# Optimization experiments

Hardware: AMD Instinct MI355X
Metric: run time of the kernel (lower is better)

Reference implementation:

```python
import jax, jax.numpy as jnp
import numpy as np

B, N_IMG, N_TXT = 8, 4096, 512
IMG_DIM, TEXT_DIM, H = 512, 768, 8
HD = IMG_DIM // H                      # 64, projection head dim
SCALE = (TEXT_DIM // H) ** -0.5        # module scales by text_head_dim^-0.5 (96)


def setup_inputs() -> dict:
    key = jax.random.key(0)
    ks = jax.random.split(key, 8)
    img_embeds = jax.random.normal(ks[0], (B, N_IMG, IMG_DIM), dtype=jnp.float32)
    text_embeds = jax.random.normal(ks[1], (B, N_TXT, TEXT_DIM), dtype=jnp.float32)
    text_attention_mask = jax.random.randint(ks[2], (B, N_TXT), 0, 2).astype(jnp.int32)
    s = 0.02
    Wq = jax.random.normal(ks[3], (IMG_DIM, IMG_DIM), dtype=jnp.float32) * s
    Wk = jax.random.normal(ks[4], (IMG_DIM, TEXT_DIM), dtype=jnp.float32) * s
    Wv = jax.random.normal(ks[5], (IMG_DIM, TEXT_DIM), dtype=jnp.float32) * s
    Wo = jax.random.normal(ks[6], (IMG_DIM, IMG_DIM), dtype=jnp.float32) * s
    bo = jnp.zeros((IMG_DIM,), dtype=jnp.float32)
    return {"img_embeds": img_embeds, "text_embeds": text_embeds,
            "text_attention_mask": text_attention_mask,
            "Wq": Wq, "Wk": Wk, "Wv": Wv, "Wo": Wo, "bo": bo}


def reference(img_embeds, text_embeds, text_attention_mask, Wq, Wk, Wv, Wo, bo):
    # projections (nn.Linear: x @ W.T), split into heads: (B, H, N, HD)
    q = (img_embeds @ Wq.T).reshape(B, N_IMG, H, HD).transpose(0, 2, 1, 3)
    k = (text_embeds @ Wk.T).reshape(B, N_TXT, H, HD).transpose(0, 2, 1, 3)
    v = (text_embeds @ Wv.T).reshape(B, N_TXT, H, HD).transpose(0, 2, 1, 3)
    # scores: (B, H, N_img, N_text)
    scores = jnp.einsum('bhid,bhjd->bhij', q, k) * SCALE
    mask = (text_attention_mask != 0)[:, None, None, :]  # (B,1,1,N_text)
    scores = jnp.where(mask, scores, -jnp.inf)
    probs = jax.nn.softmax(scores, axis=-1)
    attended = jnp.einsum('bhij,bhjd->bhid', probs, v)    # (B,H,N_img,HD)
    attended = attended.transpose(0, 2, 1, 3).reshape(B, N_IMG, IMG_DIM)
    return attended @ Wo.T + bo
```

## Files before the change

### kernel.cpp

```cpp
#include <hip/hip_runtime.h>
#include <hip/hip_bf16.h>
#include <cstdint>

#define NB   8
#define NIMG 4096
#define NTXT 512
#define DIMG 512
#define DTXT 768
#define NH   8
#define HD   64
#define SCALE 0.102062072615966f

typedef __attribute__((ext_vector_type(8))) short          s16x8;
typedef __attribute__((ext_vector_type(4))) unsigned short u16x4;
typedef __attribute__((ext_vector_type(4))) float          f32x4;
typedef unsigned short u16;
typedef unsigned int   u32;

union U8 { s16x8 v; u16 u[8]; };

__device__ __forceinline__ u16 f2bf(float f) {
  u32 u = __float_as_uint(f);
  u += 0x7fffu + ((u >> 16) & 1u);
  return (u16)(u >> 16);
}
__device__ __forceinline__ s16x8 cvt8(float4 a, float4 b) {
  U8 t;
  t.u[0]=f2bf(a.x); t.u[1]=f2bf(a.y); t.u[2]=f2bf(a.z); t.u[3]=f2bf(a.w);
  t.u[4]=f2bf(b.x); t.u[5]=f2bf(b.y); t.u[6]=f2bf(b.z); t.u[7]=f2bf(b.w);
  return t.v;
}

__global__ void convk(const float* __restrict__ in, u16* __restrict__ out, int n8) {
  int i = blockIdx.x * 256 + threadIdx.x;
  const int stride = gridDim.x * 256;
  for (; i < n8; i += stride) {
    float4 a = ((const float4*)in)[2 * i];
    float4 b = ((const float4*)in)[2 * i + 1];
    ((s16x8*)out)[i] = cvt8(a, b);
  }
}

__device__ __forceinline__ void gld16(const u16* g, u16* l) {
  __builtin_amdgcn_global_load_lds((const __attribute__((address_space(1))) u32*)g,
                                   (__attribute__((address_space(3))) u32*)l, 16, 0, 0);
}

template<int EPI, int NPER>
__global__ __launch_bounds__(256, 2)
void gemm_bf(const u16* __restrict__ A, const u16* __restrict__ W,
             const float* __restrict__ bias, void* __restrict__ Cp,
             const int N, const int K) {
  __shared__ u16 As[128 * 64];
  __shared__ u16 Bs[128 * 64];
  const int tid = threadIdx.x, lane = tid & 63, w = tid >> 6;
  const int l15 = lane & 15, l4 = lane >> 4;
  const int wm = (w >> 1) * 64, wn = (w & 1) * 64;
  const int m0 = blockIdx.y * 128, n0 = blockIdx.x * 128;
  const int srow = lane >> 3, schk = lane & 7;

  f32x4 acc[4][4] = {};

  for (int k0 = 0; k0 < K; k0 += 64) {
    __syncthreads();
#pragma unroll
    for (int i = 0; i < 4; ++i) {
      const int rg  = (w * 4 + i) * 8;
      const int row = rg + srow;
      const int sc  = schk ^ (row & 7);
      gld16(A + (size_t)(m0 + row) * K + k0 + sc * 8, &As[rg * 64]);
      gld16(W + (size_t)(n0 + row) * K + k0 + sc * 8, &Bs[rg * 64]);
    }
    __syncthreads();
#pragma unroll
    for (int ks = 0; ks < 2; ++ks) {
      s16x8 af[4], bw[4];
#pragma unroll
      for (int mf = 0; mf < 4; ++mf) {
        const int row = wm + mf * 16 + l15;
        af[mf] = *(const s16x8*)&As[row * 64 + (((ks * 4 + l4) ^ (row & 7)) << 3)];
      }
#pragma unroll
      for (int nf = 0; nf < 4; ++nf) {
        const int row = wn + nf * 16 + l15;
        bw[nf] = *(const s16x8*)&Bs[row * 64 + (((ks * 4 + l4) ^ (row & 7)) << 3)];
      }
#pragma unroll
      for (int mf = 0; mf < 4; ++mf)
#pragma unroll
        for (int nf = 0; nf < 4; ++nf)
          acc[mf][nf] = __builtin_amdgcn_mfma_f32_16x16x32_bf16(af[mf], bw[nf], acc[mf][nf], 0, 0, 0);
    }
  }

#pragma unroll
  for (int mf = 0; mf < 4; ++mf)
#pragma unroll
    for (int nf = 0; nf < 4; ++nf)
#pragma unroll
      for (int r = 0; r < 4; ++r) {
        const int grow = m0 + wm + mf * 16 + l4 * 4 + r;
        const int gcol = n0 + wn + nf * 16 + l15;
        const float v = acc[mf][nf][r];
        if constexpr (EPI == 2) {
          ((float*)Cp)[(size_t)grow * N + gcol] = v + bias[gcol];
        } else {
          const int bb = grow / NPER, nr = grow % NPER;
          const int hh = gcol >> 6, dd = gcol & 63;
          ((u16*)Cp)[((size_t)(bb * NH + hh) * NPER + nr) * HD + dd] = f2bf(v);
        }
      }
}

__global__ __launch_bounds__(256, 2)
void gemm_kv(const float* __restrict__ txt, const float* __restrict__ Wk,
             const float* __restrict__ Wv, u16* __restrict__ Kbf,
             u16* __restrict__ Vtw) {
  constexpr int K = DTXT;
  __shared__ u16 As[128 * 64];
  __shared__ u16 Bs[128 * 64];
  const int tid = threadIdx.x, lane = tid & 63, w = tid >> 6;
  const int l15 = lane & 15, l4 = lane >> 4;
  const int wm = (w >> 1) * 64, wn = (w & 1) * 64;
  const float* W = (blockIdx.x < 4) ? Wk : Wv;
  const int n0 = (blockIdx.x & 3) * 128;
  const int m0 = blockIdx.y * 128;

  f32x4 acc[4][4] = {};

  for (int k0 = 0; k0 < K; k0 += 64) {
    __syncthreads();
#pragma unroll
    for (int p = 0; p < 4; ++p) {
      const int q = tid + p * 256;
      const int row = q >> 3, c = q & 7;
      const int dst = row * 64 + ((c ^ (row & 7)) << 3);
      const float* sa = txt + (size_t)(m0 + row) * K + k0 + c * 8;
      *(s16x8*)&As[dst] = cvt8(*(const float4*)sa, *(const float4*)(sa + 4));
      const float* sw = W + (size_t)(n0 + row) * K + k0 + c * 8;
      *(s16x8*)&Bs[dst] = cvt8(*(const float4*)sw, *(const float4*)(sw + 4));
    }
    __syncthreads();
#pragma unroll
    for (int ks = 0; ks < 2; ++ks) {
      s16x8 af[4], bw[4];
#pragma unroll
      for (int mf = 0; mf < 4; ++mf) {
        const int row = wm + mf * 16 + l15;
        af[mf] = *(const s16x8*)&As[row * 64 + (((ks * 4 + l4) ^ (row & 7)) << 3)];
      }
#pragma unroll
      for (int nf = 0; nf < 4; ++nf) {
        const int row = wn + nf * 16 + l15;
        bw[nf] = *(const s16x8*)&Bs[row * 64 + (((ks * 4 + l4) ^ (row & 7)) << 3)];
      }
#pragma unroll
      for (int mf = 0; mf < 4; ++mf)
#pragma unroll
        for (int nf = 0; nf < 4; ++nf)
          acc[mf][nf] = __builtin_amdgcn_mfma_f32_16x16x32_bf16(af[mf], bw[nf], acc[mf][nf], 0, 0, 0);
    }
  }

#pragma unroll
  for (int mf = 0; mf < 4; ++mf)
#pragma unroll
    for (int nf = 0; nf < 4; ++nf)
#pragma unroll
      for (int r = 0; r < 4; ++r) {
        const int grow = m0 + wm + mf * 16 + l4 * 4 + r;
        const int gcol = n0 + wn + nf * 16 + l15;
        const int bb = grow >> 9, nr = grow & 511;
        const int hh = gcol >> 6, dd = gcol & 63;
        const u16 v = f2bf(acc[mf][nf][r]);
        if (blockIdx.x < 4)
          Kbf[((size_t)(bb * NH + hh) * NTXT + nr) * HD + dd] = v;
        else
          Vtw[((size_t)(bb * NH + hh) * HD + dd) * NTXT + nr] = v;
      }
}

__global__ __launch_bounds__(256, 2)
void attn_k(const u16* __restrict__ Qbf,
            const u16* __restrict__ Kbf,
            const u16* __restrict__ Vt,
            const int* __restrict__ msk,
            u16* __restrict__ Abf) {
  __shared__ u16 Plds[4][32 * 64];
  const int blk = blockIdx.x;
  const int qt = blk & 31, bh = blk >> 5;
  const int b = bh >> 3, h = bh & 7;
  const int tid = threadIdx.x, lane = tid & 63, w = tid >> 6;
  const int l15 = lane & 15, l4 = lane >> 4;
  const int sbase = lane & 48;

  const u16* Qb = Qbf + (size_t)bh * NIMG * HD;
  const u16* Kb = Kbf + (size_t)bh * NTXT * HD;
  const u16* Vb = Vt  + (size_t)bh * HD * NTXT;
  const int* mb = msk + b * NTXT;
  const int qrow0 = qt * 128 + w * 32;

  s16x8 aq[2][2];
#pragma unroll
  for (int nfq = 0; nfq < 2; ++nfq)
#pragma unroll
    for (int ks = 0; ks < 2; ++ks)
      aq[nfq][ks] = *(const s16x8*)(Qb + (size_t)(qrow0 + nfq * 16 + l15) * HD + ks * 32 + l4 * 8);

  f32x4 o[2][4] = {};
  float mst[2] = {-1e30f, -1e30f}, lst[2] = {0.f, 0.f};

  for (int t = 0; t < 8; ++t) {
    const int j0 = t * 64;
    s16x8 bk[4][2];
#pragma unroll
    for (int mfk = 0; mfk < 4; ++mfk)
#pragma unroll
      for (int ks = 0; ks < 2; ++ks)
        bk[mfk][ks] = *(const s16x8*)(Kb + (size_t)(j0 + mfk * 16 + l15) * HD + ks * 32 + l4 * 8);

    f32x4 st[4][2] = {};
#pragma unroll
    for (int ks = 0; ks < 2; ++ks)
#pragma unroll
      for (int mfk = 0; mfk < 4; ++mfk)
#pragma unroll
        for (int nfq = 0; nfq < 2; ++nfq)
          st[mfk][nfq] = __builtin_amdgcn_mfma_f32_16x16x32_bf16(bk[mfk][ks], aq[nfq][ks], st[mfk][nfq], 0, 0, 0);

    s16x8 bv[4][2];
#pragma unroll
    for (int hf = 0; hf < 4; ++hf)
#pragma unroll
      for (int ks = 0; ks < 2; ++ks)
        bv[hf][ks] = *(const s16x8*)(Vb + (size_t)(hf * 16 + l15) * NTXT + j0 + ks * 32 + l4 * 8);

    float madd[4][4];
#pragma unroll
    for (int mfk = 0; mfk < 4; ++mfk) {
      const int4 mm = *(const int4*)(mb + j0 + mfk * 16 + l4 * 4);
      madd[mfk][0] = mm.x ? 0.f : -1e30f;
      madd[mfk][1] = mm.y ? 0.f : -1e30f;
      madd[mfk][2] = mm.z ? 0.f : -1e30f;
      madd[mfk][3] = mm.w ? 0.f : -1e30f;
    }

#pragma unroll
    for (int nfq = 0; nfq < 2; ++nfq) {
      float nm = -1e30f;
#pragma unroll
      for (int mfk = 0; mfk < 4; ++mfk)
#pragma unroll
        for (int r = 0; r < 4; ++r) {
          const float sv = st[mfk][nfq][r] * SCALE + madd[mfk][r];
          st[mfk][nfq][r] = sv;
          nm = fmaxf(nm, sv);
        }
      nm = fmaxf(nm, __shfl_xor(nm, 16));
      nm = fmaxf(nm, __shfl_xor(nm, 32));
      const float mn = fmaxf(mst[nfq], nm);
      const float alpha = __expf(mst[nfq] - mn);
      mst[nfq] = mn;
      float ps = 0.f;
#pragma unroll
      for (int mfk = 0; mfk < 4; ++mfk)
#pragma unroll
        for (int r = 0; r < 4; ++r) {
          const float p = __expf(st[mfk][nfq][r] - mn);
          st[mfk][nfq][r] = p;
          ps += p;
        }
      ps += __shfl_xor(ps, 16);
      ps += __shfl_xor(ps, 32);
      lst[nfq] = lst[nfq] * alpha + ps;

      float ar[4];
#pragma unroll
      for (int r = 0; r < 4; ++r) ar[r] = __shfl(alpha, sbase + l4 * 4 + r);
#pragma unroll
      for (int hf = 0; hf < 4; ++hf)
#pragma unroll
        for (int r = 0; r < 4; ++r) o[nfq][hf][r] *= ar[r];

      const int q = nfq * 16 + l15;
      const int E = (q & 7) << 1;
#pragma unroll
      for (int mfk = 0; mfk < 4; ++mfk) {
        u16x4 pk;
        pk[0] = f2bf(st[mfk][nfq][0]); pk[1] = f2bf(st[mfk][nfq][1]);
        pk[2] = f2bf(st[mfk][nfq][2]); pk[3] = f2bf(st[mfk][nfq][3]);
        const int c8 = mfk * 4 + l4;
        *(u16x4*)((char*)&Plds[w][0] + q * 128 + (((c8) ^ E) << 3)) = pk;
      }
    }
    asm volatile("" ::: "memory");

#pragma unroll
    for (int mfq = 0; mfq < 2; ++mfq) {
      const int q = mfq * 16 + l15;
      const int E = (q & 7) << 1;
      s16x8 pa[2];
#pragma unroll
      for (int ks = 0; ks < 2; ++ks)
        pa[ks] = *(const s16x8*)((const char*)&Plds[w][0] + q * 128 + (((ks * 8 + l4 * 2) ^ E) << 3));
#pragma unroll
      for (int hf = 0; hf < 4; ++hf)
#pragma unroll
        for (int ks = 0; ks < 2; ++ks)
          o[mfq][hf] = __builtin_amdgcn_mfma_f32_16x16x32_bf16(pa[ks], bv[hf][ks], o[mfq][hf], 0, 0, 0);
    }
  }

#pragma unroll
  for (int nfq = 0; nfq < 2; ++nfq) {
    const float rl = 1.f / lst[nfq];
    float rr[4];
#pragma unroll
    for (int r = 0; r < 4; ++r) rr[r] = __shfl(rl, sbase + l4 * 4 + r);
#pragma unroll
    for (int hf = 0; hf < 4; ++hf)
#pragma unroll
      for (int r = 0; r < 4; ++r) {
        const int qrow = qrow0 + nfq * 16 + l4 * 4 + r;
        const int col = h * 64 + hf * 16 + l15;
        Abf[((size_t)b * NIMG + qrow) * DIMG + col] = f2bf(o[nfq][hf][r] * rr[r]);
      }
  }
}

extern "C" void kernel_launch(void* const* d_in, const int* in_sizes, int n_in,
                              void* d_out, int out_size, void* d_ws, size_t ws_size,
                              hipStream_t stream) {
  const float* img  = (const float*)d_in[0];
  const float* txt  = (const float*)d_in[1];
  const int*   mask = (const int*)d_in[2];
  const float* Wq   = (const float*)d_in[3];
  const float* Wk   = (const float*)d_in[4];
  const float* Wv   = (const float*)d_in[5];
  const float* Wo   = (const float*)d_in[6];
  const float* bo   = (const float*)d_in[7];
  float* out = (float*)d_out;

  char* ws = (char*)d_ws;
  u16* imgBf = (u16*)ws;
  u16* Qbf   = (u16*)(ws + 33554432);
  u16* Kbf   = (u16*)(ws + 67108864);
  u16* Vtw   = (u16*)(ws + 71303168);
  u16* WqBf  = (u16*)(ws + 75497472);
  u16* WoBf  = (u16*)(ws + 76021760);

  convk<<<2048, 256, 0, stream>>>(img, imgBf, NB * NIMG * DIMG / 8);
  convk<<<128,  256, 0, stream>>>(Wq, WqBf, DIMG * DIMG / 8);
  convk<<<128,  256, 0, stream>>>(Wo, WoBf, DIMG * DIMG / 8);

  gemm_bf<0, NIMG><<<dim3(4, 256), 256, 0, stream>>>(imgBf, WqBf, nullptr, Qbf, DIMG, DIMG);
  gemm_kv<<<dim3(8, 32), 256, 0, stream>>>(txt, Wk, Wv, Kbf, Vtw);
  attn_k<<<dim3(NB * NH * (NIMG / 128)), 256, 0, stream>>>(Qbf, Kbf, Vtw, mask, imgBf);
  gemm_bf<2, 1><<<dim3(4, 256), 256, 0, stream>>>(imgBf, WoBf, bo, out, DIMG, DIMG);
}
```

Measured before the change: 377.5 us.

## Prefetch next K tile in attention, remap GEMM block order, raise occupancy

The attention kernel now double-buffers K fragments in registers, loading the next 64-key tile right after the current score MFMAs so the global load latency overlaps the softmax and PV work. The two GEMM kernels remap their block IDs with an interleave of stride 8, likely to spread neighbouring tiles across XCDs or improve L2 reuse. Attention launch bounds rise from 2 to 4 waves per EU, which caps registers and may cause spills given the extra prefetch buffers.

```diff
diff --git a/kernel.cpp b/kernel.cpp
--- a/kernel.cpp
+++ b/kernel.cpp
@@ -56,7 +56,10 @@
   const int tid = threadIdx.x, lane = tid & 63, w = tid >> 6;
   const int l15 = lane & 15, l4 = lane >> 4;
   const int wm = (w >> 1) * 64, wn = (w & 1) * 64;
-  const int m0 = blockIdx.y * 128, n0 = blockIdx.x * 128;
+  const int nwg  = gridDim.x * gridDim.y;
+  const int orig = blockIdx.y * gridDim.x + blockIdx.x;
+  const int nid  = (orig & 7) * (nwg >> 3) + (orig >> 3);
+  const int m0 = (nid >> 2) * 128, n0 = (nid & 3) * 128;
   const int srow = lane >> 3, schk = lane & 7;
 
   f32x4 acc[4][4] = {};
@@ -122,9 +125,12 @@
   const int tid = threadIdx.x, lane = tid & 63, w = tid >> 6;
   const int l15 = lane & 15, l4 = lane >> 4;
   const int wm = (w >> 1) * 64, wn = (w & 1) * 64;
-  const float* W = (blockIdx.x < 4) ? Wk : Wv;
-  const int n0 = (blockIdx.x & 3) * 128;
-  const int m0 = blockIdx.y * 128;
+  const int orig = blockIdx.y * 8 + blockIdx.x;
+  const int nid  = (orig & 7) * 32 + (orig >> 3);
+  const int bx = nid & 7, by = nid >> 3;
+  const float* W = (bx < 4) ? Wk : Wv;
+  const int n0 = (bx & 3) * 128;
+  const int m0 = by * 128;
 
   f32x4 acc[4][4] = {};
 
@@ -173,14 +179,14 @@
         const int bb = grow >> 9, nr = grow & 511;
         const int hh = gcol >> 6, dd = gcol & 63;
         const u16 v = f2bf(acc[mf][nf][r]);
-        if (blockIdx.x < 4)
+        if (bx < 4)
           Kbf[((size_t)(bb * NH + hh) * NTXT + nr) * HD + dd] = v;
         else
           Vtw[((size_t)(bb * NH + hh) * HD + dd) * NTXT + nr] = v;
       }
 }
 
-__global__ __launch_bounds__(256, 2)
+__global__ __launch_bounds__(256, 4)
 void attn_k(const u16* __restrict__ Qbf,
             const u16* __restrict__ Kbf,
             const u16* __restrict__ Vt,
@@ -210,15 +216,14 @@
   f32x4 o[2][4] = {};
   float mst[2] = {-1e30f, -1e30f}, lst[2] = {0.f, 0.f};
 
-  for (int t = 0; t < 8; ++t) {
-    const int j0 = t * 64;
-    s16x8 bk[4][2];
-#pragma unroll
-    for (int mfk = 0; mfk < 4; ++mfk)
-#pragma unroll
-      for (int ks = 0; ks < 2; ++ks)
-        bk[mfk][ks] = *(const s16x8*)(Kb + (size_t)(j0 + mfk * 16 + l15) * HD + ks * 32 + l4 * 8);
-
+  s16x8 bkA[4][2], bkB[4][2];
+#pragma unroll
+  for (int mfk = 0; mfk < 4; ++mfk)
+#pragma unroll
+    for (int ks = 0; ks < 2; ++ks)
+      bkA[mfk][ks] = *(const s16x8*)(Kb + (size_t)(mfk * 16 + l15) * HD + ks * 32 + l4 * 8);
+
+  auto tile = [&](int j0, s16x8 (&bkc)[4][2], s16x8 (&bkn)[4][2], int pj0, bool pf) {
     f32x4 st[4][2] = {};
 #pragma unroll
     for (int ks = 0; ks < 2; ++ks)
@@ -226,7 +231,15 @@
       for (int mfk = 0; mfk < 4; ++mfk)
 #pragma unroll
         for (int nfq = 0; nfq < 2; ++nfq)
-          st[mfk][nfq] = __builtin_amdgcn_mfma_f32_16x16x32_bf16(bk[mfk][ks], aq[nfq][ks], st[mfk][nfq], 0, 0, 0);
+          st[mfk][nfq] = __builtin_amdgcn_mfma_f32_16x16x32_bf16(bkc[mfk][ks], aq[nfq][ks], st[mfk][nfq], 0, 0, 0);
+
+    if (pf) {
+#pragma unroll
+      for (int mfk = 0; mfk < 4; ++mfk)
+#pragma unroll
+        for (int ks = 0; ks < 2; ++ks)
+          bkn[mfk][ks] = *(const s16x8*)(Kb + (size_t)(pj0 + mfk * 16 + l15) * HD + ks * 32 + l4 * 8);
+    }
 
     s16x8 bv[4][2];
 #pragma unroll
@@ -309,6 +322,11 @@
         for (int ks = 0; ks < 2; ++ks)
           o[mfq][hf] = __builtin_amdgcn_mfma_f32_16x16x32_bf16(pa[ks], bv[hf][ks], o[mfq][hf], 0, 0, 0);
     }
+  };
+
+  for (int t = 0; t < 8; t += 2) {
+    tile(t * 64,       bkA, bkB, (t + 1) * 64, true);
+    tile((t + 1) * 64, bkB, bkA, (t + 2) * 64, t < 6);
   }
 
 #pragma unroll
```

After: 552.5 us. 46.4% more time.
